# Kernel optimization log

Hardware: AMD Instinct MI355X
Metric: run time of the kernel (lower is better)

The kernel has to match this reference:

```python
import jax, jax.numpy as jnp
import numpy as np

B, T, D = 4, 2048, 768
E, F, K = 8, 4 * 768, 2


def setup_inputs() -> dict:
    key = jax.random.key(0)
    ks = jax.random.split(key, 5)
    s = 0.02
    return {
        "x": jax.random.normal(ks[0], (B, T, D), dtype=jnp.float32),
        "Wg": jax.random.normal(ks[1], (D, E), dtype=jnp.float32) * s,
        "bg": jnp.zeros((E,), dtype=jnp.float32),
        "W1": jax.random.normal(ks[2], (E, D, F), dtype=jnp.float32) * s,
        "b1": jnp.zeros((E, F), dtype=jnp.float32),
        "W2": jax.random.normal(ks[3], (E, F, D), dtype=jnp.float32) * s,
        "b2": jnp.zeros((E, D), dtype=jnp.float32),
    }


def reference(x, Wg, bg, W1, b1, W2, b2):
    b, t, d = x.shape
    x_flat = x.reshape(-1, d)                      # [N, D]
    n = x_flat.shape[0]

    # Router: softmax over expert logits, take top-2
    gates = jax.nn.softmax(x_flat @ Wg + bg, axis=-1)   # [N, E]
    topk_g, topk_i = jax.lax.top_k(gates, K)            # [N, K]

    # Combine weights: zero for non-selected experts -> math identical to
    # masked dispatch in the torch loop (out = sum_k gate_k * expert_{idx_k}(x))
    combine = jnp.zeros((n, W1.shape[0]), dtype=gates.dtype)
    combine = combine.at[jnp.arange(n)[:, None], topk_i].add(topk_g)  # [N, E]

    # Per-expert MLP applied densely, then weighted combine (zero weights
    # kill non-selected experts' contributions)
    h = jnp.einsum('nd,edf->enf', x_flat, W1) + b1[:, None, :]  # [E, N, F]
    h = jax.nn.gelu(h, approximate=False)                        # torch nn.GELU = exact
    y = jnp.einsum('enf,efd->end', h, W2) + b2[:, None, :]       # [E, N, D]
    out = jnp.einsum('ne,end->nd', combine, y)                   # [N, D]
    return out.reshape(b, t, d)
```

## Files before the change

kernel.cpp:

```cpp
#include <hip/hip_runtime.h>
#include <hip/hip_bf16.h>


#define N_TOK 8192
#define D_DIM 768
#define E_EXP 8
#define F_DIM 3072
#define CAP   8192
#define NT_MAX 136

typedef __attribute__((ext_vector_type(8))) short s8v;
typedef __attribute__((ext_vector_type(4))) float f4v;
typedef unsigned short u16;
typedef unsigned int   u32;
typedef unsigned long long u64;

static __device__ __forceinline__ u16 f2bf(float f) {
    u32 u = __float_as_uint(f);
    return (u16)((u + 0x7fffu + ((u >> 16) & 1u)) >> 16);
}
static __device__ __forceinline__ float bf2f(u16 v) {
    return __uint_as_float((u32)v << 16);
}
static __device__ __forceinline__ float gelu_fast(float v) {
    const float av = fabsf(v);
    const float z  = av * 0.70710678118654752440f;
    const float t  = __builtin_amdgcn_rcpf(fmaf(0.3275911f, z, 1.0f));
    const float w  = __builtin_amdgcn_exp2f(-z * z * 1.4426950408889634f);
    float p = fmaf(1.061405429f, t, -1.453152027f);
    p = fmaf(p, t,  1.421413741f);
    p = fmaf(p, t, -0.284496736f);
    p = fmaf(p, t,  0.254829592f);
    p = p * t;
    const float E = 1.0f - p * w;
    return 0.5f * (v + av * E);
}
static __device__ __forceinline__ void gld_lds16(const u16* g, u16* l) {
    __builtin_amdgcn_global_load_lds(
        (const __attribute__((address_space(1))) void*)g,
        (__attribute__((address_space(3))) void*)l, 16, 0, 0);
}

__device__ __forceinline__ void pack_w_body(
    const float* __restrict__ src, u16* __restrict__ dst,
    int rt, int kc64, int e, int K1, int M2, int KC2, int TR, int ntm)
{
    __shared__ float ls[64][132];
    const float* se = src + (size_t)e * K1 * M2;
    const int tid = threadIdx.x;

    const int kr = tid >> 2, mq = tid & 3;
    const float* srow = se + (size_t)(kc64 * 64 + kr) * M2 + rt * 128 + mq * 32;
    #pragma unroll
    for (int it = 0; it < 8; ++it)
        *(float4*)&ls[kr][mq * 32 + it * 4] = *(const float4*)(srow + it * 4);
    __syncthreads();

    u16* dt_ = dst + ((size_t)(e * ntm + (rt * 128) / TR) * KC2 + kc64 * 2)
                     * ((size_t)TR * 32)
                   + (size_t)((rt * 128) % TR) * 32;
    const int rr = tid >> 1, hf = tid & 1;
    u16* dc = dt_ + (size_t)hf * TR * 32;
    const int row = ((rt * 128) % TR) + rr;
    #pragma unroll
    for (int j = 0; j < 4; ++j) {
        union { s8v v; u16 u[8]; } o;
        #pragma unroll
        for (int jj = 0; jj < 8; ++jj)
            o.u[jj] = f2bf(ls[hf * 32 + j * 8 + jj][rr]);
        *(s8v*)&dc[(size_t)rr * 32 + ((j ^ ((row >> 1) & 3)) * 8)] = o.v;
    }
}

__global__ __launch_bounds__(256) void prep_kernel(
    const float* __restrict__ x, const float* __restrict__ Wg,
    const float* __restrict__ bg, const float* __restrict__ W1,
    const float* __restrict__ W2, u32* __restrict__ rec_idx,
    float2* __restrict__ rec_g, u16* __restrict__ w1g,
    u16* __restrict__ w2g, int* __restrict__ counts)
{
    const int bid = blockIdx.x;
    if (bid == 0 && threadIdx.x < E_EXP) counts[threadIdx.x] = 0;

    if (bid < 2048) {
        const int wave = threadIdx.x >> 6;
        const int lane = threadIdx.x & 63;
        const int t = bid * 4 + wave;

        float acc[8];
        #pragma unroll
        for (int e = 0; e < 8; ++e) acc[e] = 0.f;

        const float* xrow = x + (size_t)t * D_DIM + lane * 12;
        #pragma unroll
        for (int i = 0; i < 3; ++i) {
            float4 xv = *(const float4*)(xrow + i * 4);
            float xs[4] = {xv.x, xv.y, xv.z, xv.w};
            #pragma unroll
            for (int j = 0; j < 4; ++j) {
                const int d = lane * 12 + i * 4 + j;
                const float4 w0 = *(const float4*)(Wg + (size_t)d * 8);
                const float4 w1 = *(const float4*)(Wg + (size_t)d * 8 + 4);
                acc[0] += xs[j] * w0.x;  acc[1] += xs[j] * w0.y;
                acc[2] += xs[j] * w0.z;  acc[3] += xs[j] * w0.w;
                acc[4] += xs[j] * w1.x;  acc[5] += xs[j] * w1.y;
                acc[6] += xs[j] * w1.z;  acc[7] += xs[j] * w1.w;
            }
        }
        #pragma unroll
        for (int e = 0; e < 8; ++e) {
            float v = acc[e];
            #pragma unroll
            for (int off = 32; off > 0; off >>= 1) v += __shfl_xor(v, off, 64);
            acc[e] = v + bg[e];
        }
        if (lane == 0) {
            float mx = acc[0];
            #pragma unroll
            for (int e = 1; e < 8; ++e) mx = fmaxf(mx, acc[e]);
            float p[8], s = 0.f;
            #pragma unroll
            for (int e = 0; e < 8; ++e) { p[e] = expf(acc[e] - mx); s += p[e]; }
            const float inv = 1.f / s;
            #pragma unroll
            for (int e = 0; e < 8; ++e) p[e] *= inv;

            int i0 = 0; float g0 = p[0];
            #pragma unroll
            for (int e = 1; e < 8; ++e) if (p[e] > g0) { g0 = p[e]; i0 = e; }
            int i1 = -1; float g1 = -1.f;
            #pragma unroll
            for (int e = 0; e < 8; ++e) if (e != i0 && p[e] > g1) { g1 = p[e]; i1 = e; }

            rec_idx[t] = (u32)i0 | ((u32)i1 << 4);
            rec_g[t] = make_float2(g0, g1);
        }
    } else if (bid < 4352) {
        const int id = bid - 2048;
        const int e = id / 288, rem = id - e * 288;
        const int rt = rem / 12, kc = rem - rt * 12;
        pack_w_body(W1, w1g, rt, kc, e, D_DIM, F_DIM, 24, 256, 12);
    } else {
        const int id = bid - 4352;
        const int e = id / 288, rem = id - e * 288;
        const int rt = rem / 48, kc = rem - rt * 48;
        pack_w_body(W2, w2g, rt, kc, e, F_DIM, D_DIM, 96, 128, 6);
    }
}

__global__ __launch_bounds__(256) void moe_scatter(
    const u32* __restrict__ rec_idx, const float2* __restrict__ rec_g,
    int* __restrict__ counts, int* __restrict__ tokbuf,
    float* __restrict__ gatebuf)
{
    const int t = blockIdx.x * 256 + threadIdx.x;
    const int lane = threadIdx.x & 63;
    const u32 pk = rec_idx[t];
    const int i0 = pk & 15, i1 = (pk >> 4) & 15;
    const float2 g = rec_g[t];
    const u64 lmask = ((u64)1 << lane) - 1;

    #pragma unroll
    for (int e = 0; e < 8; ++e) {
        const u64 m0 = __ballot(i0 == e);
        const u64 m1 = __ballot(i1 == e);
        const int c0 = __popcll(m0);
        const int total = c0 + __popcll(m1);
        if (total > 0) {
            int base = 0;
            if (lane == 0) base = atomicAdd(&counts[e], total);
            base = __shfl(base, 0, 64);
            if (i0 == e) {
                const int p = base + __popcll(m0 & lmask);
                tokbuf[(size_t)e * CAP + p] = 2 * t;
                gatebuf[(size_t)e * CAP + p] = g.x;
            }
            if (i1 == e) {
                const int p = base + c0 + __popcll(m1 & lmask);
                tokbuf[(size_t)e * CAP + p] = 2 * t + 1;
                gatebuf[(size_t)e * CAP + p] = g.y;
            }
        }
    }
}

__global__ void scan_kernel(const int* __restrict__ counts,
                            int* __restrict__ te, int* __restrict__ tb,
                            int* __restrict__ ntile) {
    if (threadIdx.x == 0) {
        int nt = 0;
        for (int e = 0; e < E_EXP; ++e)
            for (int k = 0; k * 128 < counts[e]; ++k) {
                te[nt] = e; tb[nt] = k * 128; ++nt;
            }
        *ntile = nt;
    }
}

__global__ __launch_bounds__(256) void pack_x(
    const float* __restrict__ x, const int* __restrict__ counts,
    const int* __restrict__ te, const int* __restrict__ tb,
    const int* __restrict__ ntile, const int* __restrict__ tokbuf,
    u16* __restrict__ xg)
{
    const int bx = blockIdx.x, kc = blockIdx.y;
    if (bx >= *ntile) return;
    const int e = te[bx], base = tb[bx], cnt = counts[e];
    const int tid = threadIdx.x;
    const int r = tid >> 1, hf = tid & 1;
    int ent = base + r; if (ent >= cnt) ent = cnt - 1;
    const int tok = tokbuf[(size_t)e * CAP + ent] >> 1;
    const float* xr = x + (size_t)tok * D_DIM + kc * 64 + hf * 32;
    u16* xt = xg + ((size_t)bx * 24 + kc * 2 + hf) * 4096;
    #pragma unroll
    for (int j = 0; j < 4; ++j) {
        float4 a = *(const float4*)(xr + j * 8);
        float4 b = *(const float4*)(xr + j * 8 + 4);
        union { s8v v; u16 u[8]; } o;
        o.u[0] = f2bf(a.x); o.u[1] = f2bf(a.y); o.u[2] = f2bf(a.z); o.u[3] = f2bf(a.w);
        o.u[4] = f2bf(b.x); o.u[5] = f2bf(b.y); o.u[6] = f2bf(b.z); o.u[7] = f2bf(b.w);
        *(s8v*)&xt[(size_t)r * 32 + ((j ^ ((r >> 1) & 3)) * 8)] = o.v;
    }
}

__global__ __launch_bounds__(256, 2) void s1_gemm(
    const u16* __restrict__ xg, const u16* __restrict__ w1g,
    const float* __restrict__ b1, const int* __restrict__ te,
    const int* __restrict__ ntile, u16* __restrict__ hg)
{
    __shared__ u16 Als[2][8192];
    __shared__ u16 Bls[2][4096];
    const int bx = blockIdx.x, by = blockIdx.y;
    if (bx >= *ntile) return;
    const int e = te[bx];

    const int tid  = threadIdx.x;
    const int w    = tid >> 6;
    const int lane = tid & 63;
    const int wm   = w & 1, wn = w >> 1;
    const int q    = lane >> 4, ln = lane & 15;
    const int colU = (q ^ ((ln >> 1) & 3)) * 8;

    const u16* Ab = w1g + (size_t)(e * 12 + by) * 24 * 8192;
    const u16* Bb = xg  + (size_t)bx * 24 * 4096;

    f4v acc[8][4];
    #pragma unroll
    for (int mi = 0; mi < 8; ++mi)
        #pragma unroll
        for (int ni = 0; ni < 4; ++ni) acc[mi][ni] = (f4v){0.f,0.f,0.f,0.f};

    {
        const u16* A0 = Ab + w * 2048 + lane * 8;
        const u16* B0 = Bb + w * 1024 + lane * 8;
        #pragma unroll
        for (int it = 0; it < 4; ++it)
            gld_lds16(A0 + it * 512, &Als[0][w * 2048 + it * 512]);
        #pragma unroll
        for (int it = 0; it < 2; ++it)
            gld_lds16(B0 + it * 512, &Bls[0][w * 1024 + it * 512]);
    }
    __syncthreads();

    for (int s = 0; s < 24; ++s) {
        const int nxt = s + 1;
        if (nxt < 24) {
            const u16* An = Ab + (size_t)nxt * 8192 + w * 2048 + lane * 8;
            const u16* Bn = Bb + (size_t)nxt * 4096 + w * 1024 + lane * 8;
            u16* Ad = &Als[nxt & 1][w * 2048];
            u16* Bd = &Bls[nxt & 1][w * 1024];
            #pragma unroll
            for (int it = 0; it < 4; ++it) gld_lds16(An + it * 512, Ad + it * 512);
            #pragma unroll
            for (int it = 0; it < 2; ++it) gld_lds16(Bn + it * 512, Bd + it * 512);
        }
        const int cur = s & 1;
        s8v af[8], bf[4];
        #pragma unroll
        for (int mi = 0; mi < 8; ++mi)
            af[mi] = *(const s8v*)&Als[cur][(wm * 128 + mi * 16 + ln) * 32 + colU];
        #pragma unroll
        for (int ni = 0; ni < 4; ++ni)
            bf[ni] = *(const s8v*)&Bls[cur][(wn * 64 + ni * 16 + ln) * 32 + colU];
        #pragma unroll
        for (int mi = 0; mi < 8; ++mi)
            #pragma unroll
            for (int ni = 0; ni < 4; ++ni)
                acc[mi][ni] = __builtin_amdgcn_mfma_f32_16x16x32_bf16(
                    af[mi], bf[ni], acc[mi][ni], 0, 0, 0);
        __syncthreads();
    }

    const float* b1e = b1 + (size_t)e * F_DIM + by * 256;
    #pragma unroll
    for (int mi = 0; mi < 8; ++mi) {
        const int floc = wm * 128 + mi * 16 + q * 4;
        const int kc2  = by * 8 + (floc >> 5);
        const int cg   = (floc >> 3) & 3;
        const float4 bv = *(const float4*)&b1e[floc];
        #pragma unroll
        for (int ni = 0; ni < 4; ++ni) {
            const int rr = wn * 64 + ni * 16 + ln;
            u16 us[4];
            us[0] = f2bf(gelu_fast(acc[mi][ni][0] + bv.x));
            us[1] = f2bf(gelu_fast(acc[mi][ni][1] + bv.y));
            us[2] = f2bf(gelu_fast(acc[mi][ni][2] + bv.z));
            us[3] = f2bf(gelu_fast(acc[mi][ni][3] + bv.w));
            uint2 pk;
            pk.x = (u32)us[0] | ((u32)us[1] << 16);
            pk.y = (u32)us[2] | ((u32)us[3] << 16);
            *(uint2*)&hg[((size_t)bx * 96 + kc2) * 4096 +
                         (size_t)rr * 32 + ((cg ^ ((rr >> 1) & 3)) * 8) +
                         (q & 1) * 4] = pk;
        }
    }
}

__global__ __launch_bounds__(256) void s2_gemm(
    const u16* __restrict__ hg, const u16* __restrict__ w2g,
    const int* __restrict__ counts, const int* __restrict__ te,
    const int* __restrict__ tb, const int* __restrict__ ntile,
    const int* __restrict__ tokbuf, const float* __restrict__ gatebuf,
    u16* __restrict__ y)
{
    __shared__ u16 Als[2][4096];
    __shared__ u16 Bls[2][4096];
    __shared__ int   sts[128];
    __shared__ float sg[128];
    const int bx = blockIdx.x, by = blockIdx.y;
    if (bx >= *ntile) return;
    const int e = te[bx], base = tb[bx], cnt = counts[e];

    const int tid  = threadIdx.x;
    const int w    = tid >> 6;
    const int lane = tid & 63;
    const int wm   = w & 1, wn = w >> 1;
    const int q    = lane >> 4, ln = lane & 15;
    const int colU = (q ^ ((ln >> 1) & 3)) * 8;

    if (tid < 128) {
        const int ent = base + tid;
        const bool v = ent < cnt;
        sts[tid] = v ? tokbuf[(size_t)e * CAP + ent] : -1;
        sg[tid]  = v ? gatebuf[(size_t)e * CAP + ent] : 0.f;
    }

    const u16* Ab = w2g + (size_t)(e * 6 + by) * 96 * 4096;
    const u16* Bb = hg  + (size_t)bx * 96 * 4096;

    f4v acc[4][4];
    #pragma unroll
    for (int mi = 0; mi < 4; ++mi)
        #pragma unroll
        for (int ni = 0; ni < 4; ++ni) acc[mi][ni] = (f4v){0.f,0.f,0.f,0.f};

    {
        const u16* A0 = Ab + w * 1024 + lane * 8;
        const u16* B0 = Bb + w * 1024 + lane * 8;
        gld_lds16(A0,       &Als[0][w * 1024]);
        gld_lds16(A0 + 512, &Als[0][w * 1024 + 512]);
        gld_lds16(B0,       &Bls[0][w * 1024]);
        gld_lds16(B0 + 512, &Bls[0][w * 1024 + 512]);
    }
    __syncthreads();

    for (int s = 0; s < 96; ++s) {
        const int nxt = s + 1;
        if (nxt < 96) {
            const u16* An = Ab + (size_t)nxt * 4096 + w * 1024 + lane * 8;
            const u16* Bn = Bb + (size_t)nxt * 4096 + w * 1024 + lane * 8;
            u16* Ad = &Als[nxt & 1][w * 1024];
            u16* Bd = &Bls[nxt & 1][w * 1024];
            gld_lds16(An,       Ad);
            gld_lds16(An + 512, Ad + 512);
            gld_lds16(Bn,       Bd);
            gld_lds16(Bn + 512, Bd + 512);
        }
        const int cur = s & 1;
        s8v af[4], bf[4];
        #pragma unroll
        for (int mi = 0; mi < 4; ++mi)
            af[mi] = *(const s8v*)&Als[cur][(wm * 64 + mi * 16 + ln) * 32 + colU];
        #pragma unroll
        for (int ni = 0; ni < 4; ++ni)
            bf[ni] = *(const s8v*)&Bls[cur][(wn * 64 + ni * 16 + ln) * 32 + colU];
        #pragma unroll
        for (int mi = 0; mi < 4; ++mi)
            #pragma unroll
            for (int ni = 0; ni < 4; ++ni)
                acc[mi][ni] = __builtin_amdgcn_mfma_f32_16x16x32_bf16(
                    af[mi], bf[ni], acc[mi][ni], 0, 0, 0);
        __syncthreads();
    }

    #pragma unroll
    for (int ni = 0; ni < 4; ++ni) {
        const int rr = wn * 64 + ni * 16 + ln;
        const int ts = sts[rr];
        if (ts >= 0) {
            const float g = sg[rr];
            u16* yr = y + (size_t)ts * D_DIM + by * 128 + wm * 64;
            #pragma unroll
            for (int mi = 0; mi < 4; ++mi) {
                u16 us[4];
                us[0] = f2bf(g * acc[mi][ni][0]);
                us[1] = f2bf(g * acc[mi][ni][1]);
                us[2] = f2bf(g * acc[mi][ni][2]);
                us[3] = f2bf(g * acc[mi][ni][3]);
                uint2 pk;
                pk.x = (u32)us[0] | ((u32)us[1] << 16);
                pk.y = (u32)us[2] | ((u32)us[3] << 16);
                *(uint2*)&yr[mi * 16 + q * 4] = pk;
            }
        }
    }
}

__global__ __launch_bounds__(256) void combine_kernel(
    const u16* __restrict__ y, const u32* __restrict__ rec_idx,
    const float2* __restrict__ rec_g, const float* __restrict__ b2,
    float* __restrict__ out)
{
    const int gid = blockIdx.x * 256 + threadIdx.x;
    const int t = gid / 192;
    const int c = (gid - t * 192) * 4;
    const u32 pk = rec_idx[t];
    const int i0 = pk & 15, i1 = (pk >> 4) & 15;
    const float2 g = rec_g[t];
    union { uint2 p; u16 u[4]; } a, b;
    a.p = *(const uint2*)&y[(size_t)(2 * t) * D_DIM + c];
    b.p = *(const uint2*)&y[(size_t)(2 * t + 1) * D_DIM + c];
    const float4 ba = *(const float4*)&b2[(size_t)i0 * D_DIM + c];
    const float4 bb = *(const float4*)&b2[(size_t)i1 * D_DIM + c];
    float4 o;
    o.x = g.x * ba.x + g.y * bb.x + bf2f(a.u[0]) + bf2f(b.u[0]);
    o.y = g.x * ba.y + g.y * bb.y + bf2f(a.u[1]) + bf2f(b.u[1]);
    o.z = g.x * ba.z + g.y * bb.z + bf2f(a.u[2]) + bf2f(b.u[2]);
    o.w = g.x * ba.w + g.y * bb.w + bf2f(a.u[3]) + bf2f(b.u[3]);
    *(float4*)&out[(size_t)t * D_DIM + c] = o;
}

extern "C" void kernel_launch(void* const* d_in, const int* in_sizes, int n_in,
                              void* d_out, int out_size, void* d_ws, size_t ws_size,
                              hipStream_t stream) {
    const float* x  = (const float*)d_in[0];
    const float* Wg = (const float*)d_in[1];
    const float* bg = (const float*)d_in[2];
    const float* W1 = (const float*)d_in[3];
    const float* b1 = (const float*)d_in[4];
    const float* W2 = (const float*)d_in[5];
    const float* b2 = (const float*)d_in[6];
    float* out = (float*)d_out;

    char* ws = (char*)d_ws;
    size_t off = 0;
    u16* xg  = (u16*)(ws + off); off += (size_t)NT_MAX * 24 * 4096 * sizeof(u16);
    u16* w1g = (u16*)(ws + off); off += (size_t)E_EXP * F_DIM * D_DIM * sizeof(u16);
    u16* w2g = (u16*)(ws + off); off += (size_t)E_EXP * D_DIM * F_DIM * sizeof(u16);
    u16* hg  = (u16*)(ws + off); off += (size_t)NT_MAX * 96 * 4096 * sizeof(u16);
    u16* y   = (u16*)(ws + off); off += (size_t)2 * N_TOK * D_DIM * sizeof(u16);
    int* tokbuf = (int*)(ws + off);      off += (size_t)E_EXP * CAP * sizeof(int);
    float* gatebuf = (float*)(ws + off); off += (size_t)E_EXP * CAP * sizeof(float);
    u32* rec_idx = (u32*)(ws + off);     off += (size_t)N_TOK * sizeof(u32);
    float2* rec_g = (float2*)(ws + off); off += (size_t)N_TOK * sizeof(float2);
    int* counts = (int*)(ws + off);      off += 64;
    int* te     = (int*)(ws + off);      off += NT_MAX * sizeof(int);
    int* tb     = (int*)(ws + off);      off += NT_MAX * sizeof(int);
    int* ntile  = (int*)(ws + off);      off += 64;

    prep_kernel<<<6656, 256, 0, stream>>>(x, Wg, bg, W1, W2, rec_idx, rec_g,
                                          w1g, w2g, counts);
    moe_scatter<<<N_TOK / 256, 256, 0, stream>>>(rec_idx, rec_g, counts, tokbuf, gatebuf);
    scan_kernel<<<1, 64, 0, stream>>>(counts, te, tb, ntile);
    pack_x<<<dim3(NT_MAX, 12), 256, 0, stream>>>(x, counts, te, tb, ntile, tokbuf, xg);

    s1_gemm<<<dim3(NT_MAX, 12), 256, 0, stream>>>(xg, w1g, b1, te, ntile, hg);
    s2_gemm<<<dim3(NT_MAX, 6), 256, 0, stream>>>(hg, w2g, counts, te, tb, ntile,
                                                 tokbuf, gatebuf, y);
    combine_kernel<<<(N_TOK * 192) / 256, 256, 0, stream>>>(y, rec_idx, rec_g, b2, out);
}
```

Measured before the change: 529.7 us.

## Triple-buffer LDS pipeline in both expert GEMMs with explicit vmcnt waits

Both expert GEMM kernels move from double-buffered LDS loads with a __syncthreads per step to a three-stage ring. Loads run two stages ahead and the code waits with explicit s_waitcnt vmcnt counts and raw s_barrier. The MFMA block now runs under s_setprio(1), and s2_gemm gets a launch bound of 3 blocks per CU. The goal is to hide global load latency better and cut the full waitcnt drains at each barrier, at the cost of more LDS per block, which may lower occupancy in s1.

```diff
diff --git a/kernel.cpp b/kernel.cpp
--- a/kernel.cpp
+++ b/kernel.cpp
@@ -39,6 +39,13 @@
     __builtin_amdgcn_global_load_lds(
         (const __attribute__((address_space(1))) void*)g,
         (__attribute__((address_space(3))) void*)l, 16, 0, 0);
+}
+template<int N> static __device__ __forceinline__ void wait_vmcnt() {
+    asm volatile("s_waitcnt vmcnt(%0)" :: "n"(N) : "memory");
+}
+static __device__ __forceinline__ void wait_lgkm0() {
+    asm volatile("s_waitcnt lgkmcnt(0)" ::: "memory");
+    __builtin_amdgcn_sched_barrier(0);
 }
 
 __device__ __forceinline__ void pack_w_body(
@@ -223,13 +230,48 @@
     }
 }
 
+#define S1_STAGE(S, SBUF) do {                                                \
+    const u16* An_ = Ab + (size_t)(S) * 8192 + w * 2048 + lane * 8;           \
+    const u16* Bn_ = Bb + (size_t)(S) * 4096 + w * 1024 + lane * 8;           \
+    u16* Ad_ = &Als[SBUF][w * 2048];                                          \
+    u16* Bd_ = &Bls[SBUF][w * 1024];                                          \
+    gld_lds16(An_,        Ad_);                                               \
+    gld_lds16(An_ +  512, Ad_ +  512);                                        \
+    gld_lds16(An_ + 1024, Ad_ + 1024);                                        \
+    gld_lds16(An_ + 1536, Ad_ + 1536);                                        \
+    gld_lds16(Bn_,        Bd_);                                               \
+    gld_lds16(Bn_ +  512, Bd_ +  512);                                        \
+} while (0)
+
+#define S1_COMPUTE(BUF, VM) do {                                              \
+    wait_vmcnt<VM>();                                                         \
+    __builtin_amdgcn_s_barrier();                                             \
+    s8v af[8], bf[4];                                                         \
+    _Pragma("unroll")                                                         \
+    for (int mi = 0; mi < 8; ++mi)                                            \
+        af[mi] = *(const s8v*)&Als[BUF][(wm*128 + mi*16 + ln)*32 + colU];     \
+    _Pragma("unroll")                                                         \
+    for (int ni = 0; ni < 4; ++ni)                                            \
+        bf[ni] = *(const s8v*)&Bls[BUF][(wn*64 + ni*16 + ln)*32 + colU];      \
+    wait_lgkm0();                                                             \
+    __builtin_amdgcn_s_barrier();                                             \
+    __builtin_amdgcn_s_setprio(1);                                            \
+    _Pragma("unroll")                                                         \
+    for (int mi = 0; mi < 8; ++mi)                                            \
+        _Pragma("unroll")                                                     \
+        for (int ni = 0; ni < 4; ++ni)                                        \
+            acc[mi][ni] = __builtin_amdgcn_mfma_f32_16x16x32_bf16(            \
+                af[mi], bf[ni], acc[mi][ni], 0, 0, 0);                        \
+    __builtin_amdgcn_s_setprio(0);                                            \
+} while (0)
+
 __global__ __launch_bounds__(256, 2) void s1_gemm(
     const u16* __restrict__ xg, const u16* __restrict__ w1g,
     const float* __restrict__ b1, const int* __restrict__ te,
     const int* __restrict__ ntile, u16* __restrict__ hg)
 {
-    __shared__ u16 Als[2][8192];
-    __shared__ u16 Bls[2][4096];
+    __shared__ __align__(16) u16 Als[3][8192];
+    __shared__ __align__(16) u16 Bls[3][4096];
     const int bx = blockIdx.x, by = blockIdx.y;
     if (bx >= *ntile) return;
     const int e = te[bx];
@@ -250,46 +292,18 @@
         #pragma unroll
         for (int ni = 0; ni < 4; ++ni) acc[mi][ni] = (f4v){0.f,0.f,0.f,0.f};
 
-    {
-        const u16* A0 = Ab + w * 2048 + lane * 8;
-        const u16* B0 = Bb + w * 1024 + lane * 8;
-        #pragma unroll
-        for (int it = 0; it < 4; ++it)
-            gld_lds16(A0 + it * 512, &Als[0][w * 2048 + it * 512]);
-        #pragma unroll
-        for (int it = 0; it < 2; ++it)
-            gld_lds16(B0 + it * 512, &Bls[0][w * 1024 + it * 512]);
-    }
-    __syncthreads();
-
-    for (int s = 0; s < 24; ++s) {
-        const int nxt = s + 1;
-        if (nxt < 24) {
-            const u16* An = Ab + (size_t)nxt * 8192 + w * 2048 + lane * 8;
-            const u16* Bn = Bb + (size_t)nxt * 4096 + w * 1024 + lane * 8;
-            u16* Ad = &Als[nxt & 1][w * 2048];
-            u16* Bd = &Bls[nxt & 1][w * 1024];
-            #pragma unroll
-            for (int it = 0; it < 4; ++it) gld_lds16(An + it * 512, Ad + it * 512);
-            #pragma unroll
-            for (int it = 0; it < 2; ++it) gld_lds16(Bn + it * 512, Bd + it * 512);
-        }
-        const int cur = s & 1;
-        s8v af[8], bf[4];
-        #pragma unroll
-        for (int mi = 0; mi < 8; ++mi)
-            af[mi] = *(const s8v*)&Als[cur][(wm * 128 + mi * 16 + ln) * 32 + colU];
-        #pragma unroll
-        for (int ni = 0; ni < 4; ++ni)
-            bf[ni] = *(const s8v*)&Bls[cur][(wn * 64 + ni * 16 + ln) * 32 + colU];
-        #pragma unroll
-        for (int mi = 0; mi < 8; ++mi)
-            #pragma unroll
-            for (int ni = 0; ni < 4; ++ni)
-                acc[mi][ni] = __builtin_amdgcn_mfma_f32_16x16x32_bf16(
-                    af[mi], bf[ni], acc[mi][ni], 0, 0, 0);
-        __syncthreads();
-    }
+    S1_STAGE(0, 0);
+    S1_STAGE(1, 1);
+
+    #pragma unroll 1
+    for (int k = 0; k <= 18; k += 3) {
+        S1_STAGE(k + 2, 2);  S1_COMPUTE(0, 12);
+        S1_STAGE(k + 3, 0);  S1_COMPUTE(1, 12);
+        S1_STAGE(k + 4, 1);  S1_COMPUTE(2, 12);
+    }
+    S1_STAGE(23, 2);  S1_COMPUTE(0, 12);
+    S1_COMPUTE(1, 6);
+    S1_COMPUTE(2, 0);
 
     const float* b1e = b1 + (size_t)e * F_DIM + by * 256;
     #pragma unroll
@@ -316,15 +330,48 @@
     }
 }
 
-__global__ __launch_bounds__(256) void s2_gemm(
+#define S2_STAGE(S, SBUF) do {                                                \
+    const u16* An_ = Ab + (size_t)(S) * 4096 + w * 1024 + lane * 8;           \
+    const u16* Bn_ = Bb + (size_t)(S) * 4096 + w * 1024 + lane * 8;           \
+    u16* Ad_ = &Als[SBUF][w * 1024];                                          \
+    u16* Bd_ = &Bls[SBUF][w * 1024];                                          \
+    gld_lds16(An_,       Ad_);                                                \
+    gld_lds16(An_ + 512, Ad_ + 512);                                          \
+    gld_lds16(Bn_,       Bd_);                                                \
+    gld_lds16(Bn_ + 512, Bd_ + 512);                                          \
+} while (0)
+
+#define S2_COMPUTE(BUF, VM) do {                                              \
+    wait_vmcnt<VM>();                                                         \
+    __builtin_amdgcn_s_barrier();                                             \
+    s8v af[4], bf[4];                                                         \
+    _Pragma("unroll")                                                         \
+    for (int mi = 0; mi < 4; ++mi)                                            \
+        af[mi] = *(const s8v*)&Als[BUF][(wm*64 + mi*16 + ln)*32 + colU];      \
+    _Pragma("unroll")                                                         \
+    for (int ni = 0; ni < 4; ++ni)                                            \
+        bf[ni] = *(const s8v*)&Bls[BUF][(wn*64 + ni*16 + ln)*32 + colU];      \
+    wait_lgkm0();                                                             \
+    __builtin_amdgcn_s_barrier();                                             \
+    __builtin_amdgcn_s_setprio(1);                                            \
+    _Pragma("unroll")                                                         \
+    for (int mi = 0; mi < 4; ++mi)                                            \
+        _Pragma("unroll")                                                     \
+        for (int ni = 0; ni < 4; ++ni)                                        \
+            acc[mi][ni] = __builtin_amdgcn_mfma_f32_16x16x32_bf16(            \
+                af[mi], bf[ni], acc[mi][ni], 0, 0, 0);                        \
+    __builtin_amdgcn_s_setprio(0);                                            \
+} while (0)
+
+__global__ __launch_bounds__(256, 3) void s2_gemm(
     const u16* __restrict__ hg, const u16* __restrict__ w2g,
     const int* __restrict__ counts, const int* __restrict__ te,
     const int* __restrict__ tb, const int* __restrict__ ntile,
     const int* __restrict__ tokbuf, const float* __restrict__ gatebuf,
     u16* __restrict__ y)
 {
-    __shared__ u16 Als[2][4096];
-    __shared__ u16 Bls[2][4096];
+    __shared__ __align__(16) u16 Als[3][4096];
+    __shared__ __align__(16) u16 Bls[3][4096];
     __shared__ int   sts[128];
     __shared__ float sg[128];
     const int bx = blockIdx.x, by = blockIdx.y;
@@ -354,44 +401,18 @@
         #pragma unroll
         for (int ni = 0; ni < 4; ++ni) acc[mi][ni] = (f4v){0.f,0.f,0.f,0.f};
 
-    {
-        const u16* A0 = Ab + w * 1024 + lane * 8;
-        const u16* B0 = Bb + w * 1024 + lane * 8;
-        gld_lds16(A0,       &Als[0][w * 1024]);
-        gld_lds16(A0 + 512, &Als[0][w * 1024 + 512]);
-        gld_lds16(B0,       &Bls[0][w * 1024]);
-        gld_lds16(B0 + 512, &Bls[0][w * 1024 + 512]);
-    }
-    __syncthreads();
-
-    for (int s = 0; s < 96; ++s) {
-        const int nxt = s + 1;
-        if (nxt < 96) {
-            const u16* An = Ab + (size_t)nxt * 4096 + w * 1024 + lane * 8;
-            const u16* Bn = Bb + (size_t)nxt * 4096 + w * 1024 + lane * 8;
-            u16* Ad = &Als[nxt & 1][w * 1024];
-            u16* Bd = &Bls[nxt & 1][w * 1024];
-            gld_lds16(An,       Ad);
-            gld_lds16(An + 512, Ad + 512);
-            gld_lds16(Bn,       Bd);
-            gld_lds16(Bn + 512, Bd + 512);
-        }
-        const int cur = s & 1;
-        s8v af[4], bf[4];
-        #pragma unroll
-        for (int mi = 0; mi < 4; ++mi)
-            af[mi] = *(const s8v*)&Als[cur][(wm * 64 + mi * 16 + ln) * 32 + colU];
-        #pragma unroll
-        for (int ni = 0; ni < 4; ++ni)
-            bf[ni] = *(const s8v*)&Bls[cur][(wn * 64 + ni * 16 + ln) * 32 + colU];
-        #pragma unroll
-        for (int mi = 0; mi < 4; ++mi)
-            #pragma unroll
-            for (int ni = 0; ni < 4; ++ni)
-                acc[mi][ni] = __builtin_amdgcn_mfma_f32_16x16x32_bf16(
-                    af[mi], bf[ni], acc[mi][ni], 0, 0, 0);
-        __syncthreads();
-    }
+    S2_STAGE(0, 0);
+    S2_STAGE(1, 1);
+
+    #pragma unroll 1
+    for (int k = 0; k <= 90; k += 3) {
+        S2_STAGE(k + 2, 2);  S2_COMPUTE(0, 8);
+        S2_STAGE(k + 3, 0);  S2_COMPUTE(1, 8);
+        S2_STAGE(k + 4, 1);  S2_COMPUTE(2, 8);
+    }
+    S2_STAGE(95, 2);  S2_COMPUTE(0, 8);
+    S2_COMPUTE(1, 4);
+    S2_COMPUTE(2, 0);
 
     #pragma unroll
     for (int ni = 0; ni < 4; ++ni) {
```

After: 509.0 us. 3.9% less time.
